# Performance work log

Hardware: AMD Instinct MI355X
Metric: run time of the kernel (lower is better)

Reference implementation:

```python
import jax, jax.numpy as jnp
import numpy as np

H, W = 8192, 8192
KH, KW = 7, 7


def setup_inputs() -> dict:
    key = jax.random.key(0)
    kx, kw = jax.random.split(key)
    x = jax.random.normal(kx, (H, W), dtype=jnp.float32)
    weight = jax.random.normal(kw, (KH, KW), dtype=jnp.float32)
    bias = jnp.zeros((1,), dtype=jnp.float32)
    return {"x": x, "weight": weight, "bias": bias}


def reference(x, weight, bias):
    # valid 2D cross-correlation, single channel (matches corr2d)
    lhs = x[None, None, :, :]            # [1,1,H,W]
    rhs = weight[None, None, :, :]       # [O=1,I=1,kh,kw]
    y = jax.lax.conv_general_dilated(
        lhs, rhs,
        window_strides=(1, 1),
        padding="VALID",
        dimension_numbers=("NCHW", "OIHW", "NCHW"),
    )[0, 0]                               # [H-kh+1, W-kw+1]
    return y + bias[0]
```

## Files before the change

### kernel.cpp

```cpp
#include <hip/hip_runtime.h>


#define IH 8192
#define IW 8192
#define OH 8186
#define OW 8186

#define TW 64
#define TH 64
#define IN_W 70
#define IN_H 70
#define LDS_STRIDE 76
#define QPR 18

__global__ __launch_bounds__(256)
void conv7x7_kernel(const float* __restrict__ x,
                    const float* __restrict__ wgt,
                    const float* __restrict__ bias,
                    float* __restrict__ out) {
    __shared__ float tile[IN_H * LDS_STRIDE];

    const int tid = threadIdx.x;
    const int C = blockIdx.x * TW;
    const int R = blockIdx.y * TH;

    float w[49];
#pragma unroll
    for (int i = 0; i < 49; ++i) w[i] = wgt[i];
    const float b0 = bias[0];

    for (int idx = tid; idx < IN_H * QPR; idx += 256) {
        const int row = idx / QPR;
        const int qc  = idx - row * QPR;
        const int gr  = R + row;
        const int gc  = C + qc * 4;
        float4 v;
        if (gr < IH && gc + 3 < IW) {
            v = *reinterpret_cast<const float4*>(&x[(size_t)gr * IW + gc]);
        } else {
            v.x = (gr < IH && gc + 0 < IW) ? x[(size_t)gr * IW + gc + 0] : 0.0f;
            v.y = (gr < IH && gc + 1 < IW) ? x[(size_t)gr * IW + gc + 1] : 0.0f;
            v.z = (gr < IH && gc + 2 < IW) ? x[(size_t)gr * IW + gc + 2] : 0.0f;
            v.w = (gr < IH && gc + 3 < IW) ? x[(size_t)gr * IW + gc + 3] : 0.0f;
        }
        *reinterpret_cast<float4*>(&tile[row * LDS_STRIDE + qc * 4]) = v;
    }
    __syncthreads();

    const int tx = tid & 15;
    const int ty = tid >> 4;
    const int r0 = ty * 4;
    const int c0 = tx * 4;

    float acc[4][4];
#pragma unroll
    for (int o = 0; o < 4; ++o)
#pragma unroll
        for (int oc = 0; oc < 4; ++oc) acc[o][oc] = 0.0f;

#pragma unroll
    for (int ir = 0; ir < 10; ++ir) {
        const float* lrow = &tile[(r0 + ir) * LDS_STRIDE + c0];
        const float4 fa = *reinterpret_cast<const float4*>(lrow + 0);
        const float4 fb = *reinterpret_cast<const float4*>(lrow + 4);
        const float4 fc = *reinterpret_cast<const float4*>(lrow + 8);
        float f[12];
        f[0] = fa.x; f[1] = fa.y; f[2]  = fa.z; f[3]  = fa.w;
        f[4] = fb.x; f[5] = fb.y; f[6]  = fb.z; f[7]  = fb.w;
        f[8] = fc.x; f[9] = fc.y; f[10] = fc.z; f[11] = fc.w;

#pragma unroll
        for (int o = 0; o < 4; ++o) {
            const int wr = ir - o;
            if (wr < 0 || wr > 6) continue;
#pragma unroll
            for (int oc = 0; oc < 4; ++oc) {
#pragma unroll
                for (int j = 0; j < 7; ++j) {
                    acc[o][oc] += f[oc + j] * w[wr * 7 + j];
                }
            }
        }
    }

    const int orow = R + r0;
    const int ocol = C + c0;
#pragma unroll
    for (int o = 0; o < 4; ++o) {
        const int gr = orow + o;
        if (gr >= OH) continue;
        float* orow_p = &out[(size_t)gr * OW + ocol];
        if (ocol + 3 < OW) {
            float2 s0 = make_float2(acc[o][0] + b0, acc[o][1] + b0);
            float2 s1 = make_float2(acc[o][2] + b0, acc[o][3] + b0);
            *reinterpret_cast<float2*>(orow_p + 0) = s0;
            *reinterpret_cast<float2*>(orow_p + 2) = s1;
        } else {
#pragma unroll
            for (int oc = 0; oc < 4; ++oc) {
                if (ocol + oc < OW) orow_p[oc] = acc[o][oc] + b0;
            }
        }
    }
}

extern "C" void kernel_launch(void* const* d_in, const int* in_sizes, int n_in,
                              void* d_out, int out_size, void* d_ws, size_t ws_size,
                              hipStream_t stream) {
    const float* x    = (const float*)d_in[0];
    const float* wgt  = (const float*)d_in[1];
    const float* bias = (const float*)d_in[2];
    float* out = (float*)d_out;

    dim3 grid((OW + TW - 1) / TW, (OH + TH - 1) / TH);
    conv7x7_kernel<<<grid, 256, 0, stream>>>(x, wgt, bias, out);
}
```

Baseline: 566.3 us.

## Pipeline column-strip segments with double-buffered direct-to-LDS loads

Replaces one-tile-per-block with a persistent-style grid of 768 blocks. Each block walks a 64-wide column strip segment of about 1365 rows in 64-row steps. Input tiles move straight into LDS with global_load_lds into two buffers, so the next tile's load overlaps the current tile's compute. Block IDs are swizzled across XCDs, and launch bounds request 3 blocks per CU. Loads clamp row and column indices instead of branching. The change relies on __syncthreads waiting for the async LDS loads, and it doubles LDS use per block.

```diff
diff --git a/kernel.cpp b/kernel.cpp
--- a/kernel.cpp
+++ b/kernel.cpp
@@ -7,100 +7,134 @@
 #define OW 8186
 
 #define TW 64
-#define TH 64
-#define IN_W 70
-#define IN_H 70
+#define CH 64
 #define LDS_STRIDE 76
-#define QPR 18
+#define BUF_FLOATS 5376
+#define NLDSCHUNK 21
+#define NSEG 6
+#define SEG_ROWS 1365
+#define NT 22
 
-__global__ __launch_bounds__(256)
-void conv7x7_kernel(const float* __restrict__ x,
-                    const float* __restrict__ wgt,
-                    const float* __restrict__ bias,
-                    float* __restrict__ out) {
-    __shared__ float tile[IN_H * LDS_STRIDE];
+#define GLOAD_LDS(gp, lp) __builtin_amdgcn_global_load_lds( \
+    (const __attribute__((address_space(1))) void*)(gp),    \
+    (__attribute__((address_space(3))) void*)(lp), 16, 0, 0)
+
+__global__ __launch_bounds__(256, 3)
+void conv7x7_pipe(const float* __restrict__ x,
+                  const float* __restrict__ wgt,
+                  const float* __restrict__ bias,
+                  float* __restrict__ out) {
+    __shared__ float tile[2 * BUF_FLOATS];
 
     const int tid = threadIdx.x;
-    const int C = blockIdx.x * TW;
-    const int R = blockIdx.y * TH;
+
+    const int bid = blockIdx.x;
+    const int nb = (bid & 7) * 96 + (bid >> 3);
+    const int strip = nb / NSEG;
+    const int seg   = nb - strip * NSEG;
+    const int C  = strip * TW;
+    const int R0 = seg * SEG_ROWS;
+    const int Rend = (R0 + SEG_ROWS < OH) ? (R0 + SEG_ROWS) : OH;
 
     float w[49];
 #pragma unroll
     for (int i = 0; i < 49; ++i) w[i] = wgt[i];
     const float b0 = bias[0];
 
-    for (int idx = tid; idx < IN_H * QPR; idx += 256) {
-        const int row = idx / QPR;
-        const int qc  = idx - row * QPR;
-        const int gr  = R + row;
-        const int gc  = C + qc * 4;
-        float4 v;
-        if (gr < IH && gc + 3 < IW) {
-            v = *reinterpret_cast<const float4*>(&x[(size_t)gr * IW + gc]);
-        } else {
-            v.x = (gr < IH && gc + 0 < IW) ? x[(size_t)gr * IW + gc + 0] : 0.0f;
-            v.y = (gr < IH && gc + 1 < IW) ? x[(size_t)gr * IW + gc + 1] : 0.0f;
-            v.z = (gr < IH && gc + 2 < IW) ? x[(size_t)gr * IW + gc + 2] : 0.0f;
-            v.w = (gr < IH && gc + 3 < IW) ? x[(size_t)gr * IW + gc + 3] : 0.0f;
+    const int wv = tid >> 6;
+    const int ln = tid & 63;
+    int rowk[6];
+    const float* gpk[6];
+#pragma unroll
+    for (int k = 0; k < 6; ++k) {
+        const int c = wv + 4 * k;
+        const int flat = c * 256 + ln * 4;
+        const int row = flat / LDS_STRIDE;
+        const int col = flat - row * LDS_STRIDE;
+        rowk[k] = row;
+        int gcol = C + col;
+        gcol = (gcol > IW - 4) ? (IW - 4) : gcol;
+        gpk[k] = x + gcol;
+    }
+
+    auto stage = [&](int bufsel, int RB) {
+#pragma unroll
+        for (int k = 0; k < 6; ++k) {
+            const int c = wv + 4 * k;
+            if (c < NLDSCHUNK) {
+                int grow = RB + rowk[k];
+                grow = (grow > IH - 1) ? (IH - 1) : grow;
+                const float* gp = gpk[k] + (size_t)grow * IW;
+                GLOAD_LDS(gp, &tile[bufsel * BUF_FLOATS + c * 256]);
+            }
         }
-        *reinterpret_cast<float4*>(&tile[row * LDS_STRIDE + qc * 4]) = v;
-    }
-    __syncthreads();
+    };
 
     const int tx = tid & 15;
     const int ty = tid >> 4;
     const int r0 = ty * 4;
     const int c0 = tx * 4;
+    const int ocol = C + c0;
 
-    float acc[4][4];
+    stage(0, R0);
+    __syncthreads();
+
+    for (int t = 0; t < NT; ++t) {
+        const int cur = t & 1;
+
+        if (t + 1 < NT) stage(cur ^ 1, R0 + (t + 1) * CH);
+
+        float acc[4][4];
 #pragma unroll
-    for (int o = 0; o < 4; ++o)
+        for (int o = 0; o < 4; ++o)
 #pragma unroll
-        for (int oc = 0; oc < 4; ++oc) acc[o][oc] = 0.0f;
+            for (int oc = 0; oc < 4; ++oc) acc[o][oc] = 0.0f;
+
+        const float* base = &tile[cur * BUF_FLOATS + r0 * LDS_STRIDE + c0];
+#pragma unroll
+        for (int ir = 0; ir < 10; ++ir) {
+            const float4 fa = *reinterpret_cast<const float4*>(base + ir * LDS_STRIDE + 0);
+            const float4 fb = *reinterpret_cast<const float4*>(base + ir * LDS_STRIDE + 4);
+            const float4 fc = *reinterpret_cast<const float4*>(base + ir * LDS_STRIDE + 8);
+            float f[12];
+            f[0] = fa.x; f[1] = fa.y; f[2]  = fa.z; f[3]  = fa.w;
+            f[4] = fb.x; f[5] = fb.y; f[6]  = fb.z; f[7]  = fb.w;
+            f[8] = fc.x; f[9] = fc.y; f[10] = fc.z; f[11] = fc.w;
 
 #pragma unroll
-    for (int ir = 0; ir < 10; ++ir) {
-        const float* lrow = &tile[(r0 + ir) * LDS_STRIDE + c0];
-        const float4 fa = *reinterpret_cast<const float4*>(lrow + 0);
-        const float4 fb = *reinterpret_cast<const float4*>(lrow + 4);
-        const float4 fc = *reinterpret_cast<const float4*>(lrow + 8);
-        float f[12];
-        f[0] = fa.x; f[1] = fa.y; f[2]  = fa.z; f[3]  = fa.w;
-        f[4] = fb.x; f[5] = fb.y; f[6]  = fb.z; f[7]  = fb.w;
-        f[8] = fc.x; f[9] = fc.y; f[10] = fc.z; f[11] = fc.w;
-
+            for (int o = 0; o < 4; ++o) {
+                const int wr = ir - o;
+                if (wr < 0 || wr > 6) continue;
 #pragma unroll
-        for (int o = 0; o < 4; ++o) {
-            const int wr = ir - o;
-            if (wr < 0 || wr > 6) continue;
+                for (int oc = 0; oc < 4; ++oc) {
 #pragma unroll
-            for (int oc = 0; oc < 4; ++oc) {
-#pragma unroll
-                for (int j = 0; j < 7; ++j) {
-                    acc[o][oc] += f[oc + j] * w[wr * 7 + j];
+                    for (int j = 0; j < 7; ++j) {
+                        acc[o][oc] += f[oc + j] * w[wr * 7 + j];
+                    }
                 }
             }
         }
-    }
 
-    const int orow = R + r0;
-    const int ocol = C + c0;
+        const int RB = R0 + t * CH;
 #pragma unroll
-    for (int o = 0; o < 4; ++o) {
-        const int gr = orow + o;
-        if (gr >= OH) continue;
-        float* orow_p = &out[(size_t)gr * OW + ocol];
-        if (ocol + 3 < OW) {
-            float2 s0 = make_float2(acc[o][0] + b0, acc[o][1] + b0);
-            float2 s1 = make_float2(acc[o][2] + b0, acc[o][3] + b0);
-            *reinterpret_cast<float2*>(orow_p + 0) = s0;
-            *reinterpret_cast<float2*>(orow_p + 2) = s1;
-        } else {
+        for (int o = 0; o < 4; ++o) {
+            const int gr = RB + r0 + o;
+            if (gr >= Rend) continue;
+            float* orow_p = &out[(size_t)gr * OW + ocol];
+            if (ocol + 3 < OW) {
+                *reinterpret_cast<float2*>(orow_p + 0) =
+                    make_float2(acc[o][0] + b0, acc[o][1] + b0);
+                *reinterpret_cast<float2*>(orow_p + 2) =
+                    make_float2(acc[o][2] + b0, acc[o][3] + b0);
+            } else {
 #pragma unroll
-            for (int oc = 0; oc < 4; ++oc) {
-                if (ocol + oc < OW) orow_p[oc] = acc[o][oc] + b0;
+                for (int oc = 0; oc < 4; ++oc) {
+                    if (ocol + oc < OW) orow_p[oc] = acc[o][oc] + b0;
+                }
             }
         }
+
+        __syncthreads();
     }
 }
 
@@ -112,6 +146,5 @@
     const float* bias = (const float*)d_in[2];
     float* out = (float*)d_out;
 
-    dim3 grid((OW + TW - 1) / TW, (OH + TH - 1) / TH);
-    conv7x7_kernel<<<grid, 256, 0, stream>>>(x, wgt, bias, out);
+    conv7x7_pipe<<<dim3(128 * NSEG), 256, 0, stream>>>(x, wgt, bias, out);
 }
```

Result: slower. 725.9 us (+28.2%).

## Persistent band blocks with double-buffered async global-to-LDS column chunk loads

Applied to the files above, without the earlier changes.

Each block now owns a 64-row band and walks 8 column chunks of 128 outputs. Chunks are staged into double-buffered LDS with global_load_lds, so loading the next chunk overlaps compute on the current one. The per-thread tile grows to 8x4 outputs, which cuts halo reloads of LDS rows relative to the FMAs, and block IDs are swizzled for cache locality. Costs are more registers and LDS with launch bounds set for 2 blocks per CU, plus a sync per chunk and clamped edge loads.

```diff
diff --git a/kernel.cpp b/kernel.cpp
--- a/kernel.cpp
+++ b/kernel.cpp
@@ -6,101 +6,130 @@
 #define OH 8186
 #define OW 8186
 
-#define TW 64
-#define TH 64
-#define IN_W 70
-#define IN_H 70
-#define LDS_STRIDE 76
-#define QPR 18
+#define BANDH 64
+#define TROWS 70
+#define CW 128
+#define TCOLS 136
+#define NCH 8
+#define SEGW (CW * NCH)
+#define NLC 38
+#define BUF_FLOATS (NLC * 256)
 
-__global__ __launch_bounds__(256)
-void conv7x7_kernel(const float* __restrict__ x,
-                    const float* __restrict__ wgt,
-                    const float* __restrict__ bias,
-                    float* __restrict__ out) {
-    __shared__ float tile[IN_H * LDS_STRIDE];
+__global__ __launch_bounds__(256, 2)
+void conv7x7_band(const float* __restrict__ x,
+                  const float* __restrict__ wgt,
+                  const float* __restrict__ bias,
+                  float* __restrict__ out) {
+    __shared__ float tile[2 * BUF_FLOATS];
 
     const int tid = threadIdx.x;
-    const int C = blockIdx.x * TW;
-    const int R = blockIdx.y * TH;
+
+    const int bid = blockIdx.x;
+    const int g   = bid & 511;
+    const int grp = bid >> 9;
+    const int nb  = grp * 512 + (g & 7) * 64 + (g >> 3);
+    const int band = nb >> 3;
+    const int hseg = nb & 7;
+    const int R  = band * BANDH;
+    const int CB = hseg * SEGW;
 
     float w[49];
 #pragma unroll
     for (int i = 0; i < 49; ++i) w[i] = wgt[i];
     const float b0 = bias[0];
 
-    for (int idx = tid; idx < IN_H * QPR; idx += 256) {
-        const int row = idx / QPR;
-        const int qc  = idx - row * QPR;
-        const int gr  = R + row;
-        const int gc  = C + qc * 4;
-        float4 v;
-        if (gr < IH && gc + 3 < IW) {
-            v = *reinterpret_cast<const float4*>(&x[(size_t)gr * IW + gc]);
-        } else {
-            v.x = (gr < IH && gc + 0 < IW) ? x[(size_t)gr * IW + gc + 0] : 0.0f;
-            v.y = (gr < IH && gc + 1 < IW) ? x[(size_t)gr * IW + gc + 1] : 0.0f;
-            v.z = (gr < IH && gc + 2 < IW) ? x[(size_t)gr * IW + gc + 2] : 0.0f;
-            v.w = (gr < IH && gc + 3 < IW) ? x[(size_t)gr * IW + gc + 3] : 0.0f;
+    const int wv = tid >> 6;
+    const int ln = tid & 63;
+    unsigned rowbyte[10];
+    int colk[10];
+#pragma unroll
+    for (int k = 0; k < 10; ++k) {
+        const int c = wv + 4 * k;
+        const int flat = c * 256 + ln * 4;
+        const int row = flat / TCOLS;
+        const int col = flat - row * TCOLS;
+        int grow = R + row;
+        if (grow > IH - 1) grow = IH - 1;
+        rowbyte[k] = (unsigned)grow * (unsigned)(IW * 4);
+        colk[k] = col;
+    }
+
+    auto stage = [&](int bufsel, int Cc) {
+#pragma unroll
+        for (int k = 0; k < 10; ++k) {
+            const int c = wv + 4 * k;
+            if (c < NLC) {
+                int gcol = Cc + colk[k];
+                if (gcol > IW - 4) gcol = IW - 4;
+                const char* gp = (const char*)x + rowbyte[k] + (unsigned)gcol * 4u;
+                __builtin_amdgcn_global_load_lds(
+                    (const __attribute__((address_space(1))) void*)gp,
+                    (__attribute__((address_space(3))) void*)
+                        &tile[bufsel * BUF_FLOATS + c * 256],
+                    16, 0, 0);
+            }
         }
-        *reinterpret_cast<float4*>(&tile[row * LDS_STRIDE + qc * 4]) = v;
-    }
+    };
+
+    const int tx = tid & 31;
+    const int ty = tid >> 5;
+    const int r0 = ty * 8;
+    const int orow0 = R + r0;
+
+    stage(0, CB);
     __syncthreads();
 
-    const int tx = tid & 15;
-    const int ty = tid >> 4;
-    const int r0 = ty * 4;
-    const int c0 = tx * 4;
+    for (int t = 0; t < NCH; ++t) {
+        const int cur = t & 1;
+        if (t + 1 < NCH) stage(cur ^ 1, CB + (t + 1) * CW);
 
-    float acc[4][4];
+        float acc[8][4];
 #pragma unroll
-    for (int o = 0; o < 4; ++o)
+        for (int o = 0; o < 8; ++o)
 #pragma unroll
-        for (int oc = 0; oc < 4; ++oc) acc[o][oc] = 0.0f;
+            for (int oc = 0; oc < 4; ++oc) acc[o][oc] = b0;
+
+        const float* base = &tile[cur * BUF_FLOATS + r0 * TCOLS + tx * 4];
+#pragma unroll
+        for (int ir = 0; ir < 14; ++ir) {
+            const float4 fa = *reinterpret_cast<const float4*>(base + ir * TCOLS + 0);
+            const float4 fb = *reinterpret_cast<const float4*>(base + ir * TCOLS + 4);
+            const float4 fc = *reinterpret_cast<const float4*>(base + ir * TCOLS + 8);
+            float f[12];
+            f[0] = fa.x; f[1] = fa.y; f[2]  = fa.z; f[3]  = fa.w;
+            f[4] = fb.x; f[5] = fb.y; f[6]  = fb.z; f[7]  = fb.w;
+            f[8] = fc.x; f[9] = fc.y; f[10] = fc.z; f[11] = fc.w;
 
 #pragma unroll
-    for (int ir = 0; ir < 10; ++ir) {
-        const float* lrow = &tile[(r0 + ir) * LDS_STRIDE + c0];
-        const float4 fa = *reinterpret_cast<const float4*>(lrow + 0);
-        const float4 fb = *reinterpret_cast<const float4*>(lrow + 4);
-        const float4 fc = *reinterpret_cast<const float4*>(lrow + 8);
-        float f[12];
-        f[0] = fa.x; f[1] = fa.y; f[2]  = fa.z; f[3]  = fa.w;
-        f[4] = fb.x; f[5] = fb.y; f[6]  = fb.z; f[7]  = fb.w;
-        f[8] = fc.x; f[9] = fc.y; f[10] = fc.z; f[11] = fc.w;
-
+            for (int o = 0; o < 8; ++o) {
+                const int wr = ir - o;
+                if (wr < 0 || wr > 6) continue;
 #pragma unroll
-        for (int o = 0; o < 4; ++o) {
-            const int wr = ir - o;
-            if (wr < 0 || wr > 6) continue;
+                for (int oc = 0; oc < 4; ++oc) {
 #pragma unroll
-            for (int oc = 0; oc < 4; ++oc) {
-#pragma unroll
-                for (int j = 0; j < 7; ++j) {
-                    acc[o][oc] += f[oc + j] * w[wr * 7 + j];
+                    for (int j = 0; j < 7; ++j) {
+                        acc[o][oc] += f[oc + j] * w[wr * 7 + j];
+                    }
                 }
             }
         }
-    }
 
-    const int orow = R + r0;
-    const int ocol = C + c0;
+        const int ocol = CB + t * CW + tx * 4;
+        const bool p0 = (ocol + 1) < OW;
+        const bool p1 = (ocol + 3) < OW;
 #pragma unroll
-    for (int o = 0; o < 4; ++o) {
-        const int gr = orow + o;
-        if (gr >= OH) continue;
-        float* orow_p = &out[(size_t)gr * OW + ocol];
-        if (ocol + 3 < OW) {
-            float2 s0 = make_float2(acc[o][0] + b0, acc[o][1] + b0);
-            float2 s1 = make_float2(acc[o][2] + b0, acc[o][3] + b0);
-            *reinterpret_cast<float2*>(orow_p + 0) = s0;
-            *reinterpret_cast<float2*>(orow_p + 2) = s1;
-        } else {
-#pragma unroll
-            for (int oc = 0; oc < 4; ++oc) {
-                if (ocol + oc < OW) orow_p[oc] = acc[o][oc] + b0;
+        for (int o = 0; o < 8; ++o) {
+            const int gr = orow0 + o;
+            if (gr < OH) {
+                float* p = out + (size_t)gr * OW + ocol;
+                if (p0) *reinterpret_cast<float2*>(p + 0) =
+                    make_float2(acc[o][0], acc[o][1]);
+                if (p1) *reinterpret_cast<float2*>(p + 2) =
+                    make_float2(acc[o][2], acc[o][3]);
             }
         }
+
+        __syncthreads();
     }
 }
 
@@ -112,6 +141,5 @@
     const float* bias = (const float*)d_in[2];
     float* out = (float*)d_out;
 
-    dim3 grid((OW + TW - 1) / TW, (OH + TH - 1) / TH);
-    conv7x7_kernel<<<grid, 256, 0, stream>>>(x, wgt, bias, out);
+    conv7x7_band<<<dim3(128 * 8), 256, 0, stream>>>(x, wgt, bias, out);
 }
```

After: 553.1 us. 2.3% less time.

## Replace LDS tiling with direct global float4 loads and larger per-thread tiles

Applied to the files above, without the earlier changes.

Drops the shared-memory tile and barrier, so each thread reads its input rows straight from global memory with float4 loads and relies on cache for the overlap between neighbouring threads. Each thread now computes 8x4 outputs instead of 4x4, which spreads every loaded row across more output rows. Weights and bias are made wave-uniform through readfirstlane, and the bias is folded into the accumulator's starting value. Column and row indices are clamped rather than guarded at the edges. The cost is more global and L1 traffic from overlapping reads, plus higher register pressure under the occupancy hint of 6 blocks.

```diff
diff --git a/kernel.cpp b/kernel.cpp
--- a/kernel.cpp
+++ b/kernel.cpp
@@ -6,75 +6,65 @@
 #define OH 8186
 #define OW 8186
 
-#define TW 64
-#define TH 64
-#define IN_W 70
-#define IN_H 70
-#define LDS_STRIDE 76
-#define QPR 18
+#define TRPT 8
+#define TCPT 4
+#define BTX 32
+#define BTY 8
+#define TILW (BTX * TCPT)
+#define TILH (BTY * TRPT)
 
-__global__ __launch_bounds__(256)
-void conv7x7_kernel(const float* __restrict__ x,
+__global__ __launch_bounds__(256, 6)
+void conv7x7_direct(const float* __restrict__ x,
                     const float* __restrict__ wgt,
                     const float* __restrict__ bias,
                     float* __restrict__ out) {
-    __shared__ float tile[IN_H * LDS_STRIDE];
+    const int tid = threadIdx.x;
+    const int tx = tid & (BTX - 1);
+    const int ty = tid >> 5;
 
-    const int tid = threadIdx.x;
-    const int C = blockIdx.x * TW;
-    const int R = blockIdx.y * TH;
+    const int CB = blockIdx.x * TILW;
+    const int R  = blockIdx.y * TILH;
 
     float w[49];
 #pragma unroll
-    for (int i = 0; i < 49; ++i) w[i] = wgt[i];
-    const float b0 = bias[0];
+    for (int i = 0; i < 49; ++i)
+        w[i] = __uint_as_float(__builtin_amdgcn_readfirstlane(
+                   __float_as_uint(wgt[i])));
+    const float b0 = __uint_as_float(__builtin_amdgcn_readfirstlane(
+                         __float_as_uint(bias[0])));
 
-    for (int idx = tid; idx < IN_H * QPR; idx += 256) {
-        const int row = idx / QPR;
-        const int qc  = idx - row * QPR;
-        const int gr  = R + row;
-        const int gc  = C + qc * 4;
-        float4 v;
-        if (gr < IH && gc + 3 < IW) {
-            v = *reinterpret_cast<const float4*>(&x[(size_t)gr * IW + gc]);
-        } else {
-            v.x = (gr < IH && gc + 0 < IW) ? x[(size_t)gr * IW + gc + 0] : 0.0f;
-            v.y = (gr < IH && gc + 1 < IW) ? x[(size_t)gr * IW + gc + 1] : 0.0f;
-            v.z = (gr < IH && gc + 2 < IW) ? x[(size_t)gr * IW + gc + 2] : 0.0f;
-            v.w = (gr < IH && gc + 3 < IW) ? x[(size_t)gr * IW + gc + 3] : 0.0f;
-        }
-        *reinterpret_cast<float4*>(&tile[row * LDS_STRIDE + qc * 4]) = v;
-    }
-    __syncthreads();
+    const int ocol = CB + tx * TCPT;
+    const int orow0 = R + ty * TRPT;
 
-    const int tx = tid & 15;
-    const int ty = tid >> 4;
-    const int r0 = ty * 4;
-    const int c0 = tx * 4;
+    int c0 = ocol;     if (c0 > IW - 4) c0 = IW - 4;
+    int c1 = ocol + 4; if (c1 > IW - 4) c1 = IW - 4;
+    int c2 = ocol + 8; if (c2 > IW - 4) c2 = IW - 4;
 
-    float acc[4][4];
+    float acc[TRPT][TCPT];
 #pragma unroll
-    for (int o = 0; o < 4; ++o)
+    for (int o = 0; o < TRPT; ++o)
 #pragma unroll
-        for (int oc = 0; oc < 4; ++oc) acc[o][oc] = 0.0f;
+        for (int oc = 0; oc < TCPT; ++oc) acc[o][oc] = b0;
 
 #pragma unroll
-    for (int ir = 0; ir < 10; ++ir) {
-        const float* lrow = &tile[(r0 + ir) * LDS_STRIDE + c0];
-        const float4 fa = *reinterpret_cast<const float4*>(lrow + 0);
-        const float4 fb = *reinterpret_cast<const float4*>(lrow + 4);
-        const float4 fc = *reinterpret_cast<const float4*>(lrow + 8);
+    for (int ir = 0; ir < TRPT + 6; ++ir) {
+        int gr = orow0 + ir;
+        if (gr > IH - 1) gr = IH - 1;
+        const size_t rb = (size_t)gr * IW;
+        const float4 fa = *reinterpret_cast<const float4*>(x + rb + c0);
+        const float4 fb = *reinterpret_cast<const float4*>(x + rb + c1);
+        const float4 fc = *reinterpret_cast<const float4*>(x + rb + c2);
         float f[12];
         f[0] = fa.x; f[1] = fa.y; f[2]  = fa.z; f[3]  = fa.w;
         f[4] = fb.x; f[5] = fb.y; f[6]  = fb.z; f[7]  = fb.w;
         f[8] = fc.x; f[9] = fc.y; f[10] = fc.z; f[11] = fc.w;
 
 #pragma unroll
-        for (int o = 0; o < 4; ++o) {
+        for (int o = 0; o < TRPT; ++o) {
             const int wr = ir - o;
             if (wr < 0 || wr > 6) continue;
 #pragma unroll
-            for (int oc = 0; oc < 4; ++oc) {
+            for (int oc = 0; oc < TCPT; ++oc) {
 #pragma unroll
                 for (int j = 0; j < 7; ++j) {
                     acc[o][oc] += f[oc + j] * w[wr * 7 + j];
@@ -83,23 +73,17 @@
         }
     }
 
-    const int orow = R + r0;
-    const int ocol = C + c0;
+    const bool p0 = (ocol + 1) < OW;
+    const bool p1 = (ocol + 3) < OW;
 #pragma unroll
-    for (int o = 0; o < 4; ++o) {
-        const int gr = orow + o;
-        if (gr >= OH) continue;
-        float* orow_p = &out[(size_t)gr * OW + ocol];
-        if (ocol + 3 < OW) {
-            float2 s0 = make_float2(acc[o][0] + b0, acc[o][1] + b0);
-            float2 s1 = make_float2(acc[o][2] + b0, acc[o][3] + b0);
-            *reinterpret_cast<float2*>(orow_p + 0) = s0;
-            *reinterpret_cast<float2*>(orow_p + 2) = s1;
-        } else {
-#pragma unroll
-            for (int oc = 0; oc < 4; ++oc) {
-                if (ocol + oc < OW) orow_p[oc] = acc[o][oc] + b0;
-            }
+    for (int o = 0; o < TRPT; ++o) {
+        const int gr = orow0 + o;
+        if (gr < OH) {
+            float* p = out + (size_t)gr * OW + ocol;
+            if (p0) *reinterpret_cast<float2*>(p + 0) =
+                make_float2(acc[o][0], acc[o][1]);
+            if (p1) *reinterpret_cast<float2*>(p + 2) =
+                make_float2(acc[o][2], acc[o][3]);
         }
     }
 }
@@ -112,6 +96,7 @@
     const float* bias = (const float*)d_in[2];
     float* out = (float*)d_out;
 
-    dim3 grid((OW + TW - 1) / TW, (OH + TH - 1) / TH);
-    conv7x7_kernel<<<grid, 256, 0, stream>>>(x, wgt, bias, out);
+    dim3 grid((OW + TILW - 1) / TILW,
+              (OH + TILH - 1) / TILH);
+    conv7x7_direct<<<grid, dim3(256), 0, stream>>>(x, wgt, bias, out);
 }
```

After: 2.083 ms. 268% more time.
